# Kernel tuning notes

Hardware: AMD Instinct MI355X
Metric: run time of the kernel (lower is better)

## Reference

```python
import jax, jax.numpy as jnp
import numpy as np

B, Q, P = 8, 300, 5
RS, QS, CS, NC = 256, 768, 768, 396
HW = [64, 32, 16, 8]
POOL = [32, 16, 8, 4]
THR = 0.2


def _ln(x, g, b, eps=1e-5):
    m = x.mean(-1, keepdims=True)
    v = ((x - m) ** 2).mean(-1, keepdims=True)
    return (x - m) / jnp.sqrt(v + eps) * g + b


def _avgpool(x, oh, ow):
    # exact adaptive avg pool (output divides input)
    b, c, h, w = x.shape
    return x.reshape(b, c, oh, h // oh, ow, w // ow).mean((3, 5))


def setup_inputs() -> dict:
    key = jax.random.key(0)
    ks = jax.random.split(key, 40)
    inp = {}
    inp['pred_logits'] = jax.random.normal(ks[0], (B, Q, P), dtype=jnp.float32)
    inp['pred_boxes'] = jax.random.uniform(ks[1], (B, Q, 4), dtype=jnp.float32)
    inp['hs'] = jax.random.normal(ks[2], (B, Q, RS), dtype=jnp.float32)
    for s in range(4):
        inp[f'feat{s}'] = jax.random.normal(ks[3 + s], (B, 256, HW[s], HW[s]), dtype=jnp.float32)
        inp[f'pos{s}'] = jax.random.normal(ks[7 + s], (B, 256, HW[s], HW[s]), dtype=jnp.float32)
        inp[f'mask{s}'] = jax.random.bernoulli(ks[11 + s], 0.15, (B, HW[s], HW[s]))
        inp[f'convW{s}'] = jax.random.normal(ks[15 + s], (CS, 256), dtype=jnp.float32) * 0.02
        inp[f'convb{s}'] = jnp.zeros((CS,), jnp.float32)
        inp[f'lng{s}'] = jnp.ones((CS,), jnp.float32)
        inp[f'lnb{s}'] = jnp.zeros((CS,), jnp.float32)
    inp['learnable_query'] = jax.random.normal(ks[19], (P + 1, QS), dtype=jnp.float32)
    inp['Wq'] = jax.random.normal(ks[20], (RS, QS), dtype=jnp.float32) * 0.02
    inp['bq'] = jnp.zeros((QS,), jnp.float32)
    inp['qng'] = jnp.ones((QS,), jnp.float32)
    inp['qnb'] = jnp.zeros((QS,), jnp.float32)
    inp['W1'] = jax.random.normal(ks[21], (QS, QS), dtype=jnp.float32) * 0.02
    inp['b1'] = jnp.zeros((QS,), jnp.float32)
    inp['W2'] = jax.random.normal(ks[22], (QS, NC), dtype=jnp.float32) * 0.02
    inp['b2'] = jnp.zeros((NC,), jnp.float32)
    return inp


def _forward(pred_logits, pred_boxes, hs,
             feats, poss, masks, convWs, convbs, lngs, lnbs,
             learnable_query, Wq, bq, qng, qnb, W1, b1, W2, b2):
    del pred_boxes  # selected in the original but never used
    b = hs.shape[0]
    prob = jax.nn.sigmoid(pred_logits)                       # (B,Q,P)
    # per-prompt membership: logit_i > thr (implies max > thr)
    m = (prob > THR).astype(hs.dtype)                        # (B,Q,P)
    cnt = m.sum(1)                                           # (B,P)
    ssum = jnp.einsum('bqp,bqd->bpd', m, hs)                 # segment-sum over queries
    pooled = jnp.where(cnt[..., None] > 0,
                       ssum / jnp.maximum(cnt, 1.0)[..., None], 0.0)  # (B,P,RS)
    proj = pooled @ Wq + bq                                  # (B,P,QS)
    any_sel = jnp.any(prob.max(-1) > THR, axis=1)            # (B,)
    # if no query passed the global gate, prompt_hs is zeros WITHOUT projection
    prompt_hs = jnp.where(any_sel[:, None, None], proj, 0.0)
    prompt_query = learnable_query[1:] + prompt_hs           # (B,P,QS)
    cls_query = jnp.broadcast_to(learnable_query[0][None, None, :], (b, 1, QS))
    query_tokens = jnp.concatenate([cls_query, prompt_query], axis=1)
    query_tokens = _ln(query_tokens, qng, qnb)               # (B,P+1,QS)

    tokens = []
    for s in range(4):
        mask_f = masks[s][:, None, :, :].astype(feats[s].dtype)   # (B,1,H,W)
        x = (feats[s] + poss[s]) * (1.0 - mask_f)                 # masked_fill
        ctx = jnp.einsum('bchw,oc->bohw', x, convWs[s]) + convbs[s][None, :, None, None]
        p = _avgpool(ctx, POOL[s], POOL[s])
        mp = jnp.clip(_avgpool(1.0 - mask_f, POOL[s], POOL[s]), 1e-6, None)
        p = p / mp
        t = p.reshape(b, CS, -1).transpose(0, 2, 1)               # (B,T_s,CS)
        tokens.append(_ln(t, lngs[s], lnbs[s]))
    ctx_all = jnp.concatenate(tokens, axis=1)                     # (B,1360,CS)

    # encoder stand-in: fuse context into query tokens additively
    last = query_tokens + ctx_all.mean(1)[:, None, :]
    cls_logit = last[:, 0]
    prompt_logit = last[:, 1:].mean(1)
    h = jax.nn.relu((cls_logit + prompt_logit) @ W1 + b1)
    return h @ W2 + b2                                            # (B,NC)


def reference(pred_logits, pred_boxes, hs,
              feat0, pos0, mask0, convW0, convb0, lng0, lnb0,
              feat1, pos1, mask1, convW1, convb1, lng1, lnb1,
              feat2, pos2, mask2, convW2, convb2, lng2, lnb2,
              feat3, pos3, mask3, convW3, convb3, lng3, lnb3,
              learnable_query, Wq, bq, qng, qnb, W1, b1, W2, b2):
    return _forward(pred_logits, pred_boxes, hs,
                    [feat0, feat1, feat2, feat3],
                    [pos0, pos1, pos2, pos3],
                    [mask0, mask1, mask2, mask3],
                    [convW0, convW1, convW2, convW3],
                    [convb0, convb1, convb2, convb3],
                    [lng0, lng1, lng2, lng3],
                    [lnb0, lnb1, lnb2, lnb3],
                    learnable_query, Wq, bq, qng, qnb, W1, b1, W2, b2)
```

## Files before the change

kernel.cpp:

```cpp
#include <hip/hip_runtime.h>
#include <hip/hip_bf16.h>

#define Bn 8
#define Qn 300
#define Pn 5
#define RSn 256
#define QSn 768
#define NCn 396
#define MTOT 10880
#define THRL -1.3862943611198906f

typedef __attribute__((ext_vector_type(8))) short short8;
typedef __attribute__((ext_vector_type(4))) float float4v;

__device__ inline float wred(float v){
  #pragma unroll
  for (int off = 32; off; off >>= 1) v += __shfl_xor(v, off);
  return v;
}

__device__ __forceinline__ unsigned short f2bf(float f){
  union { float f; unsigned int u; } c; c.f = f;
  return (unsigned short)((c.u + 0x7FFF + ((c.u >> 16) & 1)) >> 16);
}

__global__ __launch_bounds__(256, 4) void k_front(
    const float* cw0, const float* cw1, const float* cw2, const float* cw3,
    short* Wswz, const int* __restrict__ mk0, int* det,
    const float* __restrict__ pl, const float* __restrict__ hs,
    float* pooled, int* flags, float* ctxsum, float* outz){
  int bx = blockIdx.x;
  int t = threadIdx.x;
  if (bx < 768){
    int s = bx / 192;
    int linear = (bx % 192)*256 + t;
    int q = linear & 63, n = linear >> 6;
    const float* src = (s==0)?cw0:(s==1)?cw1:(s==2)?cw2:cw3;
    float4 f = *(const float4*)(src + (size_t)n*256 + q*4);
    int kc = q >> 3, lk = (q >> 1) & 3, e0 = (q & 1)*4;
    short* dst = Wswz + ((size_t)(s*8 + kc))*24576 + lk*6144 + n*8 + e0;
    short4 sv;
    sv.x = (short)f2bf(f.x); sv.y = (short)f2bf(f.y);
    sv.z = (short)f2bf(f.z); sv.w = (short)f2bf(f.w);
    *(short4*)dst = sv;
    return;
  }
  if (bx == 768){
    __shared__ int r0[4], r1[4];
    const int* mm = mk0 + t*32;
    int d0 = 0, d1 = 0;
    #pragma unroll 8
    for (int i = 0; i < 32; ++i){
      int v = mm[i];
      d0 |= (v != 0 && v != 1);
      d1 |= (v != 0 && v != 0x3F800000);
    }
    unsigned long long bal0 = __ballot(d0), bal1 = __ballot(d1);
    int wid = t >> 6;
    if ((t & 63) == 0){ r0[wid] = (bal0 != 0ull); r1[wid] = (bal1 != 0ull); }
    __syncthreads();
    if (t == 0){
      det[0] = r0[0] | r0[1] | r0[2] | r0[3];
      det[1] = r1[0] | r1[1] | r1[2] | r1[3];
    }
    return;
  }
  if (bx >= 821){
    int idx = ((bx - 821)*256 + t)*4;
    if (idx < Bn*NCn) *(float4*)(outz + idx) = (float4){0.f,0.f,0.f,0.f};
    return;
  }
  if (bx >= 809){
    int idx = ((bx - 809)*256 + t)*4;
    *(float4*)(ctxsum + idx) = (float4){0.f,0.f,0.f,0.f};
    return;
  }
  __shared__ float msk[Qn];
  int bb = (bx - 769) / Pn, p = (bx - 769) % Pn;
  for (int q = t; q < Qn; q += 256)
    msk[q] = (pl[(bb*Qn + q)*Pn + p] > THRL) ? 1.f : 0.f;
  __syncthreads();
  const float* hb = hs + (size_t)bb*Qn*RSn + t;
  float s0 = 0.f, s1 = 0.f, s2 = 0.f, s3 = 0.f, cnt = 0.f;
  for (int q = 0; q < Qn; q += 4){
    float m0v = msk[q], m1 = msk[q+1], m2 = msk[q+2], m3 = msk[q+3];
    cnt += m0v + m1 + m2 + m3;
    s0 = fmaf(m0v, hb[(size_t)(q  )*RSn], s0);
    s1 = fmaf(m1,  hb[(size_t)(q+1)*RSn], s1);
    s2 = fmaf(m2,  hb[(size_t)(q+2)*RSn], s2);
    s3 = fmaf(m3,  hb[(size_t)(q+3)*RSn], s3);
  }
  float ssum = (s0 + s1) + (s2 + s3);
  pooled[(bb*Pn + p)*RSn + t] = (cnt > 0.f) ? ssum / cnt : 0.f;
  if (t == 0) flags[bb*Pn + p] = (cnt > 0.f) ? 1 : 0;
}

__global__ __launch_bounds__(256, 2) void k_pgemm(
    const float* fe0, const float* po0, const void* ma0,
    const float* fe1, const float* po1, const void* ma1,
    const float* fe2, const float* po2, const void* ma2,
    const float* fe3, const float* po3, const void* ma3,
    const int* __restrict__ det, const short* __restrict__ Wswz,
    const float* cb0, const float* cb1, const float* cb2, const float* cb3,
    const float* lg0, const float* lb0, const float* lg1, const float* lb1,
    const float* lg2, const float* lb2, const float* lg3, const float* lb3,
    float* __restrict__ ctxsum,
    const float* __restrict__ lq, const float* __restrict__ Wq,
    const float* __restrict__ bq, const float* __restrict__ qng,
    const float* __restrict__ qnb, const float* __restrict__ pooled,
    const int* __restrict__ flags, float* qt){
  __shared__ short As[16*264];
  __shared__ float wls[16][4];
  __shared__ float scls[16], imls[16];
  __shared__ float lsum[4][16], lsq[4][16];
  __shared__ float pq[256];
  __shared__ float s1s[4], s2s[4];
  int blk = blockIdx.x;
  int t = threadIdx.x;

  if (blk >= 680){
    int qbx = blk - 680;
    int b = qbx / 6, j = qbx % 6;
    float v0 = lq[j*QSn + t], v1 = lq[j*QSn + t + 256], v2 = lq[j*QSn + t + 512];
    int any = flags[b*Pn] | flags[b*Pn+1] | flags[b*Pn+2] | flags[b*Pn+3] | flags[b*Pn+4];
    if (j > 0 && any){
      pq[t] = pooled[(b*Pn + (j-1))*RSn + t];
      __syncthreads();
      float a0 = 0.f, a1 = 0.f, a2 = 0.f;
      #pragma unroll 8
      for (int c = 0; c < RSn; ++c){
        float pv = pq[c];
        a0 = fmaf(pv, Wq[c*QSn + t      ], a0);
        a1 = fmaf(pv, Wq[c*QSn + t + 256], a1);
        a2 = fmaf(pv, Wq[c*QSn + t + 512], a2);
      }
      v0 += a0 + bq[t]; v1 += a1 + bq[t+256]; v2 += a2 + bq[t+512];
    }
    float sm = v0 + v1 + v2, sq = v0*v0 + v1*v1 + v2*v2;
    sm = wred(sm); sq = wred(sq);
    int wid = t >> 6, lane = t & 63;
    if (lane == 0){ s1s[wid] = sm; s2s[wid] = sq; }
    __syncthreads();
    float S  = s1s[0] + s1s[1] + s1s[2] + s1s[3];
    float SQ = s2s[0] + s2s[1] + s2s[2] + s2s[3];
    float mu = S * (1.f/QSn), var = SQ * (1.f/QSn) - mu*mu;
    float rs = rsqrtf(var + 1e-5f);
    float* o = qt + (b*6 + j)*QSn;
    o[t      ] = (v0 - mu)*rs*qng[t      ] + qnb[t      ];
    o[t + 256] = (v1 - mu)*rs*qng[t + 256] + qnb[t + 256];
    o[t + 512] = (v2 - mu)*rs*qng[t + 512] + qnb[t + 512];
    return;
  }

  int m0 = blk * 16;
  int s, H, OWlog, b0;
  const float *F, *Pp; const void* M;
  const float *CB, *LG, *LB;
  if (m0 < 8192){ s=0; F=fe0; Pp=po0; M=ma0; H=64; OWlog=5; b0=m0>>10;
                  CB=cb0; LG=lg0; LB=lb0; }
  else if (m0 < 10240){ s=1; F=fe1; Pp=po1; M=ma1; H=32; OWlog=4; b0=(m0-8192)>>8;
                  CB=cb1; LG=lg1; LB=lb1; }
  else if (m0 < 10752){ s=2; F=fe2; Pp=po2; M=ma2; H=16; OWlog=3; b0=(m0-10240)>>6;
                  CB=cb2; LG=lg2; LB=lb2; }
  else { s=3; F=fe3; Pp=po3; M=ma3; H=8; OWlog=2; b0=(m0-10752)>>4;
                  CB=cb3; LG=lg3; LB=lb3; }
  int HH = H*H;
  int OWm = (H >> 1) - 1;
  int mode = (det[0] == 0) ? 0 : ((det[1] == 0) ? 2 : 1);

  int slot = t & 15;
  int gm = m0 + slot;
  int bb = b0;
  int ltl;
  if (s == 0)      ltl = gm & 1023;
  else if (s == 1) ltl = gm & 255;
  else if (s == 2) ltl = gm & 63;
  else             ltl = gm & 15;
  int ph = ltl >> OWlog, pw = ltl & OWm;
  int i00 = ph*2*H + pw*2;
  int mbase = bb*HH;

  if (t < 16){
    float w0, w1, w2, w3;
    if (mode == 0){
      const int* Mi = (const int*)M + mbase + i00;
      int2 ma = *(const int2*)(Mi);
      int2 mb = *(const int2*)(Mi + H);
      w0 = ma.x?0.f:1.f; w1 = ma.y?0.f:1.f; w2 = mb.x?0.f:1.f; w3 = mb.y?0.f:1.f;
    } else if (mode == 1){
      const unsigned char* Mb = (const unsigned char*)M + mbase + i00;
      w0 = Mb[0]?0.f:1.f; w1 = Mb[1]?0.f:1.f; w2 = Mb[H]?0.f:1.f; w3 = Mb[H+1]?0.f:1.f;
    } else {
      const float* Mf = (const float*)M + mbase + i00;
      float2 ma = *(const float2*)(Mf);
      float2 mb = *(const float2*)(Mf + H);
      w0 = 1.f-ma.x; w1 = 1.f-ma.y; w2 = 1.f-mb.x; w3 = 1.f-mb.y;
    }
    float msum = w0 + w1 + w2 + w3;
    float im = 1.f / fmaxf(msum*0.25f, 1e-6f);
    wls[t][0] = w0; wls[t][1] = w1; wls[t][2] = w2; wls[t][3] = w3;
    scls[t] = 0.25f*im; imls[t] = im;
  }
  __syncthreads();

  {
    float w0 = wls[slot][0], w1 = wls[slot][1], w2 = wls[slot][2], w3 = wls[slot][3];
    float sc = scls[slot];
    int chb = (t >> 4) * 2;
    size_t base = (size_t)(bb*256 + chb)*HH + i00;
    const float* Fp = F + base;
    const float* Pq = Pp + base;
    const int stride = 32*HH;
    #pragma unroll 2
    for (int r = 0; r < 8; ++r){
      float2 fa0 = *(const float2*)(Fp);
      float2 fb0 = *(const float2*)(Fp + H);
      float2 pa0 = *(const float2*)(Pq);
      float2 pb0 = *(const float2*)(Pq + H);
      float2 fa1 = *(const float2*)(Fp + HH);
      float2 fb1 = *(const float2*)(Fp + HH + H);
      float2 pa1 = *(const float2*)(Pq + HH);
      float2 pb1 = *(const float2*)(Pq + HH + H);
      float x0 = (fa0.x+pa0.x)*w0 + (fa0.y+pa0.y)*w1 + (fb0.x+pb0.x)*w2 + (fb0.y+pb0.y)*w3;
      float x1 = (fa1.x+pa1.x)*w0 + (fa1.y+pa1.y)*w1 + (fb1.x+pb1.x)*w2 + (fb1.y+pb1.y)*w3;
      *(unsigned int*)(&As[slot*264 + chb + r*32]) =
          (unsigned int)f2bf(x0*sc) | ((unsigned int)f2bf(x1*sc) << 16);
      Fp += stride; Pq += stride;
    }
  }
  __syncthreads();

  int wid = t >> 6, l = t & 63;
  int lm = l & 15, lk = l >> 4;
  int nfb = wid * 12;
  short8 aReg[8];
  #pragma unroll
  for (int kc = 0; kc < 8; ++kc)
    aReg[kc] = *(const short8*)(As + lm*264 + kc*32 + lk*8);

  float4v acc[12];
  #pragma unroll
  for (int nf = 0; nf < 12; ++nf) acc[nf] = (float4v){0.f,0.f,0.f,0.f};

  const short* Bb = Wswz + ((size_t)(s*8))*24576 + lk*6144 + nfb*128 + lm*8;
  short8 bCur[12], bNxt[12];
  #pragma unroll
  for (int nf = 0; nf < 12; ++nf)
    bNxt[nf] = *(const short8*)(Bb + nf*128);
  #pragma unroll
  for (int kc = 0; kc < 8; ++kc){
    #pragma unroll
    for (int nf = 0; nf < 12; ++nf) bCur[nf] = bNxt[nf];
    if (kc < 7){
      const short* bp = Bb + (kc+1)*24576;
      #pragma unroll
      for (int nf = 0; nf < 12; ++nf)
        bNxt[nf] = *(const short8*)(bp + nf*128);
    }
    #pragma unroll
    for (int nf = 0; nf < 12; ++nf)
      acc[nf] = __builtin_amdgcn_mfma_f32_16x16x32_bf16(aReg[kc], bCur[nf], acc[nf], 0, 0, 0);
  }

  float im4[4];
  #pragma unroll
  for (int r = 0; r < 4; ++r) im4[r] = imls[lk*4 + r];

  float sum[4] = {0,0,0,0}, sq[4] = {0,0,0,0};
  #pragma unroll
  for (int nf = 0; nf < 12; ++nf){
    float cbv = CB[(nfb+nf)*16 + lm];
    #pragma unroll
    for (int r = 0; r < 4; ++r){
      float p = acc[nf][r] + cbv*im4[r];
      acc[nf][r] = p;
      sum[r] += p;
      sq[r] = fmaf(p, p, sq[r]);
    }
  }
  #pragma unroll
  for (int r = 0; r < 4; ++r){
    #pragma unroll
    for (int off = 1; off < 16; off <<= 1){
      sum[r] += __shfl_xor(sum[r], off);
      sq[r]  += __shfl_xor(sq[r],  off);
    }
  }
  if (lm == 0){
    #pragma unroll
    for (int r = 0; r < 4; ++r){
      lsum[wid][lk*4 + r] = sum[r];
      lsq[wid][lk*4 + r]  = sq[r];
    }
  }
  __syncthreads();
  float mu[4], rs[4];
  #pragma unroll
  for (int r = 0; r < 4; ++r){
    int row = lk*4 + r;
    float S  = lsum[0][row] + lsum[1][row] + lsum[2][row] + lsum[3][row];
    float SQ = lsq[0][row]  + lsq[1][row]  + lsq[2][row]  + lsq[3][row];
    mu[r] = S * (1.f/768.f);
    float var = SQ * (1.f/768.f) - mu[r]*mu[r];
    rs[r] = rsqrtf(var + 1e-5f);
  }
  #pragma unroll
  for (int nf = 0; nf < 12; ++nf){
    int n = (nfb+nf)*16 + lm;
    float g = LG[n], bv = LB[n];
    float tv = 0.f;
    #pragma unroll
    for (int r = 0; r < 4; ++r)
      tv += (acc[nf][r] - mu[r]) * rs[r];
    tv = tv*g + 4.f*bv;
    tv += __shfl_xor(tv, 16); tv += __shfl_xor(tv, 32);
    if (lk == 0)
      atomicAdd(&ctxsum[b0*768 + n], tv);
  }
}

__global__ void k_hpre(const float* __restrict__ qt, const float* __restrict__ ctxsum,
                       const float* __restrict__ W1, const float* __restrict__ b1,
                       float* __restrict__ hpre){
  __shared__ float vsh[Bn][192];
  int nc = blockIdx.x % 24, kc = blockIdx.x / 24;
  int n0 = nc*32, c0 = kc*192;
  int t = threadIdx.x;
  for (int i = t; i < Bn*192; i += 256){
    int b = i / 192, cl = i - b*192;
    int c = c0 + cl;
    const float* q = qt + (size_t)b*6*768;
    float pm = q[768+c] + q[2*768+c] + q[3*768+c] + q[4*768+c] + q[5*768+c];
    vsh[b][cl] = q[c] + 0.2f*pm + ctxsum[b*768 + c]*(1.f/680.f);
  }
  __syncthreads();
  int ow = t & 31, bi = t >> 5;
  int o = n0 + ow;
  float acc = 0.f;
  const float* w = W1 + (size_t)c0*768 + o;
  #pragma unroll 4
  for (int cl = 0; cl < 192; ++cl)
    acc = fmaf(vsh[bi][cl], w[(size_t)cl*768], acc);
  if (kc == 0) acc += b1[o];
  atomicAdd(&hpre[bi*768 + o], acc);
}

__global__ void k_out(const float* __restrict__ hpre, const float* __restrict__ W2,
                      const float* __restrict__ b2, float* __restrict__ out){
  __shared__ float hsh[Bn][192];
  int nc = blockIdx.x % 13, kc = blockIdx.x / 13;
  int n0 = nc*32, c0 = kc*192;
  int t = threadIdx.x;
  for (int i = t; i < Bn*192; i += 256){
    int b = i / 192, cl = i - b*192;
    hsh[b][cl] = fmaxf(hpre[b*768 + c0 + cl], 0.f);
  }
  __syncthreads();
  int ow = t & 31, bi = t >> 5;
  int o = n0 + ow;
  if (o >= NCn) return;
  float acc = 0.f;
  const float* w = W2 + (size_t)c0*NCn + o;
  #pragma unroll 4
  for (int cl = 0; cl < 192; ++cl)
    acc = fmaf(hsh[bi][cl], w[(size_t)cl*NCn], acc);
  if (kc == 0) acc += b2[o];
  atomicAdd(&out[bi*NCn + o], acc);
}

extern "C" void kernel_launch(void* const* d_in, const int* in_sizes, int n_in,
                              void* d_out, int out_size, void* d_ws, size_t ws_size,
                              hipStream_t stream){
  const float* pl = (const float*)d_in[0];
  const float* hs = (const float*)d_in[2];
  const float* feat[4]; const float* pos[4]; const void* mask[4];
  const float* cw[4]; const float* cb[4]; const float* lg[4]; const float* lb[4];
  for (int s = 0; s < 4; ++s){
    int base = 3 + 7*s;
    feat[s] = (const float*)d_in[base];
    pos[s]  = (const float*)d_in[base+1];
    mask[s] = d_in[base+2];
    cw[s]   = (const float*)d_in[base+3];
    cb[s]   = (const float*)d_in[base+4];
    lg[s]   = (const float*)d_in[base+5];
    lb[s]   = (const float*)d_in[base+6];
  }
  const float* lq  = (const float*)d_in[31];
  const float* Wq  = (const float*)d_in[32];
  const float* bq  = (const float*)d_in[33];
  const float* qng = (const float*)d_in[34];
  const float* qnb = (const float*)d_in[35];
  const float* W1  = (const float*)d_in[36];
  const float* b1  = (const float*)d_in[37];
  const float* W2  = (const float*)d_in[38];
  const float* b2  = (const float*)d_in[39];
  float* out = (float*)d_out;

  short* Wswz   = (short*)d_ws;
  float* pooled = (float*)(Wswz + (size_t)4*8*4*768*8);
  float* qt     = pooled + 40*RSn;
  float* ctxsum = qt + Bn*6*QSn;
  float* hpre   = ctxsum + Bn*QSn;
  int*   det    = (int*)(hpre + Bn*QSn);
  int*   flags  = det + 4;

  k_front<<<825, 256, 0, stream>>>(cw[0], cw[1], cw[2], cw[3], Wswz,
                                   (const int*)mask[0], det, pl, hs, pooled, flags,
                                   ctxsum, out);
  k_pgemm<<<728, 256, 0, stream>>>(feat[0], pos[0], mask[0],
                                   feat[1], pos[1], mask[1],
                                   feat[2], pos[2], mask[2],
                                   feat[3], pos[3], mask[3],
                                   det, Wswz,
                                   cb[0], cb[1], cb[2], cb[3],
                                   lg[0], lb[0], lg[1], lb[1],
                                   lg[2], lb[2], lg[3], lb[3], ctxsum,
                                   lq, Wq, bq, qng, qnb, pooled, flags, qt);
  k_hpre<<<96, 256, 0, stream>>>(qt, ctxsum, W1, b1, hpre);
  k_out<<<52, 256, 0, stream>>>(hpre, W2, b2, out);
}
```

Baseline: 269.2 us.

## Compute mask weights per thread and double-buffer MFMA operands with sched barriers

Every thread now loads its own mask weights and computes the normalisation itself. This removes the shared-memory staging and one __syncthreads before the pooling stage, at the cost of redundant mask loads across threads. The pooling loop is fully unrolled. The GEMM main loop is restructured into a ping-pong double buffer of A (from LDS) and B (from global) fragments, with sched_barrier fences so the next k-slice loads are issued before the current MFMAs. This trades some register pressure for better load/MFMA overlap.

```diff
diff --git a/kernel.cpp b/kernel.cpp
--- a/kernel.cpp
+++ b/kernel.cpp
@@ -110,8 +110,7 @@
     const float* __restrict__ qnb, const float* __restrict__ pooled,
     const int* __restrict__ flags, float* qt){
   __shared__ short As[16*264];
-  __shared__ float wls[16][4];
-  __shared__ float scls[16], imls[16];
+  __shared__ float imls[16];
   __shared__ float lsum[4][16], lsq[4][16];
   __shared__ float pq[256];
   __shared__ float s1s[4], s2s[4];
@@ -180,8 +179,8 @@
   int i00 = ph*2*H + pw*2;
   int mbase = bb*HH;
 
-  if (t < 16){
-    float w0, w1, w2, w3;
+  float w0, w1, w2, w3;
+  {
     if (mode == 0){
       const int* Mi = (const int*)M + mbase + i00;
       int2 ma = *(const int2*)(Mi);
@@ -196,22 +195,19 @@
       float2 mb = *(const float2*)(Mf + H);
       w0 = 1.f-ma.x; w1 = 1.f-ma.y; w2 = 1.f-mb.x; w3 = 1.f-mb.y;
     }
-    float msum = w0 + w1 + w2 + w3;
-    float im = 1.f / fmaxf(msum*0.25f, 1e-6f);
-    wls[t][0] = w0; wls[t][1] = w1; wls[t][2] = w2; wls[t][3] = w3;
-    scls[t] = 0.25f*im; imls[t] = im;
-  }
-  __syncthreads();
+  }
+  float msum = w0 + w1 + w2 + w3;
+  float im = 1.f / fmaxf(msum*0.25f, 1e-6f);
+  float sc = 0.25f*im;
+  if (t < 16) imls[t] = im;
 
   {
-    float w0 = wls[slot][0], w1 = wls[slot][1], w2 = wls[slot][2], w3 = wls[slot][3];
-    float sc = scls[slot];
     int chb = (t >> 4) * 2;
     size_t base = (size_t)(bb*256 + chb)*HH + i00;
     const float* Fp = F + base;
     const float* Pq = Pp + base;
     const int stride = 32*HH;
-    #pragma unroll 2
+    #pragma unroll
     for (int r = 0; r < 8; ++r){
       float2 fa0 = *(const float2*)(Fp);
       float2 fb0 = *(const float2*)(Fp + H);
@@ -233,33 +229,43 @@
   int wid = t >> 6, l = t & 63;
   int lm = l & 15, lk = l >> 4;
   int nfb = wid * 12;
-  short8 aReg[8];
-  #pragma unroll
-  for (int kc = 0; kc < 8; ++kc)
-    aReg[kc] = *(const short8*)(As + lm*264 + kc*32 + lk*8);
 
   float4v acc[12];
   #pragma unroll
   for (int nf = 0; nf < 12; ++nf) acc[nf] = (float4v){0.f,0.f,0.f,0.f};
 
-  const short* Bb = Wswz + ((size_t)(s*8))*24576 + lk*6144 + nfb*128 + lm*8;
-  short8 bCur[12], bNxt[12];
+  const short* Bbase = Wswz + ((size_t)(s*8))*24576 + lk*6144 + nfb*128 + lm*8;
+  const short* Akbase = As + lm*264 + lk*8;
+
+  short8 a0 = *(const short8*)(Akbase + 0*32);
+  short8 b0_[12];
   #pragma unroll
   for (int nf = 0; nf < 12; ++nf)
-    bNxt[nf] = *(const short8*)(Bb + nf*128);
-  #pragma unroll
-  for (int kc = 0; kc < 8; ++kc){
-    #pragma unroll
-    for (int nf = 0; nf < 12; ++nf) bCur[nf] = bNxt[nf];
-    if (kc < 7){
-      const short* bp = Bb + (kc+1)*24576;
+    b0_[nf] = *(const short8*)(Bbase + nf*128);
+  __builtin_amdgcn_sched_barrier(0);
+
+  #pragma unroll
+  for (int kc = 0; kc < 8; kc += 2){
+    short8 a1 = *(const short8*)(Akbase + (kc+1)*32);
+    short8 b1_[12];
+    #pragma unroll
+    for (int nf = 0; nf < 12; ++nf)
+      b1_[nf] = *(const short8*)(Bbase + (size_t)(kc+1)*24576 + nf*128);
+    __builtin_amdgcn_sched_barrier(0);
+    #pragma unroll
+    for (int nf = 0; nf < 12; ++nf)
+      acc[nf] = __builtin_amdgcn_mfma_f32_16x16x32_bf16(a0, b0_[nf], acc[nf], 0, 0, 0);
+
+    if (kc + 2 < 8){
+      a0 = *(const short8*)(Akbase + (kc+2)*32);
       #pragma unroll
       for (int nf = 0; nf < 12; ++nf)
-        bNxt[nf] = *(const short8*)(bp + nf*128);
-    }
+        b0_[nf] = *(const short8*)(Bbase + (size_t)(kc+2)*24576 + nf*128);
+    }
+    __builtin_amdgcn_sched_barrier(0);
     #pragma unroll
     for (int nf = 0; nf < 12; ++nf)
-      acc[nf] = __builtin_amdgcn_mfma_f32_16x16x32_bf16(aReg[kc], bCur[nf], acc[nf], 0, 0, 0);
+      acc[nf] = __builtin_amdgcn_mfma_f32_16x16x32_bf16(a1, b1_[nf], acc[nf], 0, 0, 0);
   }
 
   float im4[4];
```

New measurement: 269.7 us. No clear change (+0.2%).
